# Kernel tuning notes

Measured on AMD Instinct MI355X. Metric: run time of the kernel, lower is better.

Reference implementation:

```python
import jax, jax.numpy as jnp
import numpy as np

N_WAY = 5
K_SHOT = 5
TEMPERATURE = 1.0
NEG = -1e9  # emulates 'column does not exist' for pad columns beyond umask_length
EPS = 1e-12  # matches torch F.normalize eps


def _l2n(x, axis):
    n = jnp.sqrt(jnp.sum(x * x, axis=axis, keepdims=True))
    return x / jnp.maximum(n, EPS)


def setup_inputs() -> dict:
    key = jax.random.key(0)
    k1, k2, k3, k4, k5 = jax.random.split(key, 5)
    b, c, h, w = 4, 64, 5, 5
    q, u = 75, 100
    support_xf = jax.random.normal(k1, (b, N_WAY * K_SHOT, c, h, w), jnp.float32)
    query_xf = jax.random.normal(k2, (b, q, c, h, w), jnp.float32)
    unlabeled_xf = jax.random.normal(k3, (b, u, c, h, w), jnp.float32)
    support_y = jax.random.randint(k4, (b, N_WAY * K_SHOT), 0, N_WAY)
    query_y = jax.random.randint(k5, (b, q), 0, N_WAY)
    return {"support_xf": support_xf, "support_y": support_y, "query_xf": query_xf,
            "query_y": query_y, "unlabeled_xf": unlabeled_xf}


def _forward(support_xf, query_xf, unlabeled_xf, query_y):
    b, q, c, h, w = query_xf.shape
    M_s = K_SHOT * h * w
    unl = unlabeled_xf.reshape(b, -1, c, h, w)
    u = unl.shape[1]
    M_u = u * h * w
    # pooled unlabeled local descriptors, flattened in (u, h, w) order -> [b, c, M_u]
    unl_feat = unl.transpose(0, 2, 1, 3, 4).reshape(b, c, M_u)
    # support -> [b, n_way, c, k_shot*h*w]
    sup = support_xf.reshape(b, N_WAY, K_SHOT, c, h, w).transpose(0, 1, 3, 2, 4, 5).reshape(b, N_WAY, c, M_s)
    # cosine similarity unlabeled -> support: [b, n_way, M_u, M_s]
    u2s = jnp.einsum('bwcn,bcm->bwmn', _l2n(sup, 2), _l2n(unl_feat, 1))
    pool = u2s.transpose(0, 2, 1, 3).reshape(b, M_u, N_WAY * M_s)
    s_nearest = jnp.argmax(pool, axis=1)          # per support loc: nearest unlabeled loc
    u_nearest = jnp.argmax(pool, axis=2)          # per unlabeled loc: nearest support loc
    mutual = jnp.take_along_axis(s_nearest, u_nearest, axis=1) == jnp.arange(M_u)[None, :]  # [b, M_u]
    # class with max similarity per unlabeled location
    cls = jnp.argmax(jnp.max(u2s, axis=-1), axis=1)  # [b, M_u]
    umask = jax.nn.one_hot(cls, N_WAY, dtype=jnp.float32).transpose(0, 2, 1) \
            * mutual[:, None, :].astype(jnp.float32)  # [b, n_way, M_u]
    counts = umask.sum(-1)                          # [b, n_way]
    L = counts.max()                                # umask_length (traced)
    # stream compaction via stable argsort of the 0/1 mask (preserves original order)
    order = jnp.argsort(-umask, axis=-1)            # jnp.argsort is stable
    pts = unl_feat.transpose(0, 2, 1)               # [b, M_u, c]
    gath = jnp.take_along_axis(pts[:, None, :, :], order[..., None], axis=2)  # [b, n_way, M_u, c]
    valid = (jnp.arange(M_u)[None, None, :] < counts[:, :, None]).astype(jnp.float32)
    comp = gath * valid[..., None]                  # rows beyond count are zeros (as in torch)
    s_cat = jnp.concatenate([sup, comp.transpose(0, 1, 3, 2)], axis=-1)  # [b, n_way, c, M_s+M_u]
    M_tot = M_s + M_u
    qn = _l2n(query_xf.reshape(b, q, c, h * w), 2)
    scn = _l2n(s_cat, 2)
    sim = jnp.einsum('bqcm,bwcn->bqwmn', qn, scn)   # [b, q, n_way, M_q, M_tot]
    sim = (sim + 1.0) * 0.5                          # FourLayer_64F branch
    # columns beyond umask_length don't exist in the torch dense tensor -> exclude from maxes
    pad = jnp.arange(M_tot)[None, None, None, None, :] >= (M_s + L)
    sim = jnp.where(pad, NEG, sim)
    M_q = h * w
    qm = sim.transpose(0, 1, 3, 2, 4).reshape(b, q, M_q, N_WAY * M_tot)
    support_nearest = jnp.argmax(qm, axis=2)        # [b, q, n_way*M_tot]
    query_nearest = jnp.argmax(qm, axis=3)          # [b, q, M_q]
    g = jnp.take_along_axis(support_nearest, query_nearest, axis=2)
    q_mask = (g == jnp.arange(M_q)[None, None, :]).astype(sim.dtype)  # mutual NN mask
    query_value = (jnp.max(sim, axis=-1) * q_mask[:, :, None, :]).sum(-1)  # [b, q, n_way]
    logits = query_value.reshape(b * q, N_WAY) / TEMPERATURE
    y = query_y.reshape(b * q)
    logp = jax.nn.log_softmax(logits, axis=-1)
    loss = -jnp.take_along_axis(logp, y[:, None], axis=1).mean()
    return loss


def reference(support_xf, support_y, query_xf, query_y, unlabeled_xf):
    return _forward(support_xf, query_xf, unlabeled_xf, query_y)
```

## Files before the change

### kernel.cpp

```cpp
#include <hip/hip_runtime.h>

#define NEGINF (-1e30f)

constexpr size_t OF_UNL  = 0;
constexpr size_t OF_SUP  = OF_UNL  + (size_t)4*2500*64;
constexpr size_t OF_SUPT = OF_SUP  + (size_t)4*5*125*64;
constexpr size_t OF_QT   = OF_SUPT + (size_t)4*5*64*128;
constexpr size_t OF_ROWV = OF_QT   + (size_t)300*28*64;
constexpr size_t OF_ROWI = OF_ROWV + (size_t)4*5*8*2500;
constexpr size_t OF_CVI  = OF_ROWI + (size_t)4*5*8*2500;
constexpr size_t OF_CMP  = OF_CVI  + (size_t)4*5*125*20*2;
constexpr size_t OF_CNT  = OF_CMP  + (size_t)4*5*2500;
constexpr size_t OF_UNEAR= OF_CNT  + 20;
constexpr size_t OF_SNEAR= OF_UNEAR+ 10000;
constexpr size_t OF_BV   = OF_SNEAR+ 2500;
constexpr size_t OF_BP   = OF_BV   + 37500;
constexpr size_t OF_AMX  = OF_BP   + 37500;

typedef __attribute__((ext_vector_type(4)))  float f4s;
typedef __attribute__((ext_vector_type(16))) float f16s;

__global__ __launch_bounds__(256) void knorm(
    const float* __restrict__ sup, const float* __restrict__ qry,
    const float* __restrict__ unl,
    float* __restrict__ unl_n, float* __restrict__ sup_n,
    float* __restrict__ supT, float* __restrict__ qt)
{
    int tid = threadIdx.x;
    int lane = tid & 63, wv = tid >> 6;
    int unit = blockIdx.x * 4 + wv;

    __shared__ float ls[4][1600];
    __shared__ float scl[4][32];

    const float* src;
    float* dstT;
    float* dst2 = nullptr;
    int dst2_shot = 0;
    bool isq = false;

    if (unit < 400) {
        int b = unit / 100, u = unit % 100;
        src  = unl + (size_t)unit * 1600;
        dstT = unl_n + ((size_t)(b * 2500 + u * 25)) * 64;
    } else if (unit < 500) {
        int idx2 = unit - 400;
        int b = idx2 / 25, r = idx2 % 25;
        int w = r / 5, shot = r % 5;
        src  = sup + (size_t)(b * 25 + r) * 1600;
        dstT = sup_n + ((size_t)(b * 625 + w * 125 + shot * 25)) * 64;
        dst2 = supT + ((size_t)(b * 5 + w) * 64) * 128;
        dst2_shot = shot * 25;
    } else {
        int bq = unit - 500;
        src  = qry + (size_t)bq * 1600;
        dstT = qt + (size_t)bq * 1792;
        isq = true;
    }

    const float4* s4 = (const float4*)src;
#pragma unroll
    for (int k = 0; k < 7; ++k) {
        int idx = k * 64 + lane;
        if (idx < 400) *(float4*)&ls[wv][idx * 4] = s4[idx];
    }
    __syncthreads();

    if (lane < 25) {
        int hw = lane;
        float p[16];
#pragma unroll
        for (int sub = 0; sub < 16; ++sub) {
            float s = 0.f;
#pragma unroll
            for (int j = 0; j < 4; ++j) {
                float v = ls[wv][(sub * 4 + j) * 25 + hw];
                s += v * v;
            }
            p[sub] = s;
        }
#pragma unroll
        for (int st = 1; st < 16; st <<= 1)
#pragma unroll
            for (int i = 0; i < 16; i += 2 * st)
                p[i] = p[i] + p[i + st];
        scl[wv][hw] = 1.f / fmaxf(sqrtf(p[0]), 1e-12f);
    }
    __syncthreads();

    float4* d4 = (float4*)dstT;
#pragma unroll
    for (int k = 0; k < 7; ++k) {
        int idx = k * 64 + lane;
        if (idx < 400) {
            int f = idx * 4;
            int r_ = f >> 6;
            int c0 = f & 63;
            float m = scl[wv][r_];
            float4 o;
            o.x = ls[wv][ c0      * 25 + r_] * m;
            o.y = ls[wv][(c0 + 1) * 25 + r_] * m;
            o.z = ls[wv][(c0 + 2) * 25 + r_] * m;
            o.w = ls[wv][(c0 + 3) * 25 + r_] * m;
            d4[idx] = o;
        }
    }
    if (isq) {
        if (lane < 48) d4[400 + lane] = make_float4(0.f, 0.f, 0.f, 0.f);
    }
    if (dst2) {
#pragma unroll
        for (int k = 0; k < 25; ++k) {
            int idx = k * 64 + lane;
            int c = idx / 25, hw2 = idx % 25;
            dst2[(size_t)c * 128 + dst2_shot + hw2] = ls[wv][idx] * scl[wv][hw2];
        }
    }
}

#define KB2(C) { \
    f16s s0, s1; \
    asm volatile("s_load_dwordx16 %0, %[b], %c[o0]\n\t" \
                 "s_load_dwordx16 %1, %[b], %c[o1]\n\t" \
                 "s_waitcnt lgkmcnt(0)" \
                 : "=s"(s0), "=s"(s1) \
                 : [b]"s"(sbp), [o0]"i"((C)*512), [o1]"i"((C)*512+512)); \
    float2 uv = *(const float2*)&uls[ml * 66 + (C)]; \
    acc[0]  = fmaf(uv.x, s0[0],  fmaf(uv.y, s1[0],  acc[0])); \
    acc[1]  = fmaf(uv.x, s0[1],  fmaf(uv.y, s1[1],  acc[1])); \
    acc[2]  = fmaf(uv.x, s0[2],  fmaf(uv.y, s1[2],  acc[2])); \
    acc[3]  = fmaf(uv.x, s0[3],  fmaf(uv.y, s1[3],  acc[3])); \
    acc[4]  = fmaf(uv.x, s0[4],  fmaf(uv.y, s1[4],  acc[4])); \
    acc[5]  = fmaf(uv.x, s0[5],  fmaf(uv.y, s1[5],  acc[5])); \
    acc[6]  = fmaf(uv.x, s0[6],  fmaf(uv.y, s1[6],  acc[6])); \
    acc[7]  = fmaf(uv.x, s0[7],  fmaf(uv.y, s1[7],  acc[7])); \
    acc[8]  = fmaf(uv.x, s0[8],  fmaf(uv.y, s1[8],  acc[8])); \
    acc[9]  = fmaf(uv.x, s0[9],  fmaf(uv.y, s1[9],  acc[9])); \
    acc[10] = fmaf(uv.x, s0[10], fmaf(uv.y, s1[10], acc[10])); \
    acc[11] = fmaf(uv.x, s0[11], fmaf(uv.y, s1[11], acc[11])); \
    acc[12] = fmaf(uv.x, s0[12], fmaf(uv.y, s1[12], acc[12])); \
    acc[13] = fmaf(uv.x, s0[13], fmaf(uv.y, s1[13], acc[13])); \
    acc[14] = fmaf(uv.x, s0[14], fmaf(uv.y, s1[14], acc[14])); \
    acc[15] = fmaf(uv.x, s0[15], fmaf(uv.y, s1[15], acc[15])); }
#define KB8(C) KB2(C) KB2((C)+2) KB2((C)+4) KB2((C)+6)

__global__ __launch_bounds__(256) void kb(
    const float* __restrict__ unl_n, const float* __restrict__ supT,
    float* __restrict__ rowv, int* __restrict__ rowi, float* __restrict__ colvi)
{
    int bid = blockIdx.x;
    int nc = bid & 3;
    int mb = (bid >> 2) % 20;
    int bw = bid / 80;
    int b  = bw / 5;
    int tid = threadIdx.x;
    int lane = tid & 63, wv = tid >> 6;

    __shared__ float uls[128 * 66];
    __shared__ float sv_[4][32];
    __shared__ int   si_[4][32];

    int m0 = mb * 128;
    int n0 = nc * 32;

    for (int i = tid; i < 128 * 16; i += 256) {
        int row = i >> 4, c4 = (i & 15) * 4;
        int m = m0 + row;
        float4 x = make_float4(0.f, 0.f, 0.f, 0.f);
        if (m < 2500) x = *(const float4*)(unl_n + ((size_t)(b * 2500 + m)) * 64 + c4);
        *(float2*)&uls[row * 66 + c4]     = make_float2(x.x, x.y);
        *(float2*)&uls[row * 66 + c4 + 2] = make_float2(x.z, x.w);
    }
    __syncthreads();

    int ml = tid & 127;
    int m  = m0 + ml;
    int nh = tid >> 7;
    int nbase = nh * 16;
    int nbu = __builtin_amdgcn_readfirstlane(nbase);
    int nn_total = (125 - n0) < 32 ? (125 - n0) : 32;
    const float* sbp = supT + ((size_t)bw * 64) * 128 + n0 + nbu;

    float acc[16];
#pragma unroll
    for (int j = 0; j < 16; ++j) acc[j] = 0.f;

    KB8(0)  KB8(8)  KB8(16) KB8(24)
    KB8(32) KB8(40) KB8(48) KB8(56)

    int nnloc = nn_total - nbase;
    nnloc = nnloc < 0 ? 0 : (nnloc > 16 ? 16 : nnloc);
    float rbv = NEGINF; int rbi = 0;
    for (int j = 0; j < nnloc; ++j)
        if (acc[j] > rbv) { rbv = acc[j]; rbi = n0 + nbase + j; }
    if (m < 2500) {
        int ck = nc * 2 + nh;
        rowv[((size_t)bw * 8 + ck) * 2500 + m] = rbv;
        rowi[((size_t)bw * 8 + ck) * 2500 + m] = rbi;
    }

#pragma unroll
    for (int j = 0; j < 16; ++j) {
        float v = (m < 2500 && (nbase + j) < nn_total) ? acc[j] : NEGINF;
        float vm = v;
#pragma unroll
        for (int s2 = 1; s2 < 64; s2 <<= 1) vm = fmaxf(vm, __shfl_xor(vm, s2));
        unsigned long long msk = __ballot(v == vm);
        int first = __ffsll((unsigned long long)msk) - 1;
        if (lane == 0) { sv_[wv][nbase + j] = vm; si_[wv][nbase + j] = m0 + (wv & 1) * 64 + first; }
    }
    __syncthreads();
    if (tid < nn_total) {
        int w0 = (tid < 16) ? 0 : 2;
        float v = sv_[w0][tid];     int vi = si_[w0][tid];
        float v2 = sv_[w0 + 1][tid]; int i2 = si_[w0 + 1][tid];
        if (v2 > v || (v2 == v && i2 < vi)) { v = v2; vi = i2; }
        float* cv = colvi + ((((size_t)bw) * 125 + (n0 + tid)) * 20 + mb) * 2;
        cv[0] = v; ((int*)cv)[1] = vi;
    }
}

__global__ __launch_bounds__(64) void kmerge(
    const float* __restrict__ rowv, const int* __restrict__ rowi,
    const float* __restrict__ colvi,
    int* __restrict__ unear, int* __restrict__ snear)
{
    int it = blockIdx.x * 64 + threadIdx.x;
    if (it < 10000) {
        int b = it / 2500, m = it % 2500;
        float bv = NEGINF; int bi = 0;
#pragma unroll
        for (int w = 0; w < 5; ++w) {
#pragma unroll
            for (int ck = 0; ck < 8; ++ck) {
                size_t o = (((size_t)(b * 5 + w)) * 8 + ck) * 2500 + m;
                float v = rowv[o];
                if (v > bv) { bv = v; bi = w * 125 + rowi[o]; }
            }
        }
        unear[it] = bi;
    } else if (it < 12500) {
        int idx = it - 10000;
        const float* p = colvi + (size_t)idx * 40;
        float bv = NEGINF; int bi = 0x7fffffff;
        for (int mb2 = 0; mb2 < 20; ++mb2) {
            float v = p[mb2 * 2]; int vi = ((const int*)p)[mb2 * 2 + 1];
            if (v > bv || (v == bv && vi < bi)) { bv = v; bi = vi; }
        }
        snear[idx] = bi;
    }
}

__global__ __launch_bounds__(256) void kcmp(
    const int* __restrict__ unear, const int* __restrict__ snear,
    int* __restrict__ cmp, int* __restrict__ cntg)
{
    int p = blockIdx.x;
    int b = p / 5, way = p % 5;
    int tid = threadIdx.x, lane = tid & 63, wv = tid >> 6;
    __shared__ unsigned long long masks[40];
    __shared__ int base[40];

    for (int ch = wv; ch < 40; ch += 4) {
        int m = ch * 64 + lane;
        bool ok = false;
        if (m < 2500) {
            int un = unear[b * 2500 + m];
            ok = (un / 125 == way) && (snear[b * 625 + un] == m);
        }
        unsigned long long msk = __ballot(ok ? 1 : 0);
        if (lane == 0) masks[ch] = msk;
    }
    __syncthreads();
    if (tid == 0) {
        int s = 0;
        for (int ch = 0; ch < 40; ++ch) { base[ch] = s; s += __popcll(masks[ch]); }
        cntg[p] = s;
    }
    __syncthreads();
    for (int ch = wv; ch < 40; ch += 4) {
        unsigned long long msk = masks[ch];
        if ((msk >> lane) & 1ull) {
            int pre = __popcll(msk & ((1ull << lane) - 1ull));
            cmp[(size_t)p * 2500 + base[ch] + pre] = ch * 64 + lane;
        }
    }
}

#define QLOAD(CG, Q0,Q1,Q2,Q3,Q4,Q5,Q6) \
  asm volatile( \
    "s_load_dwordx4 %0, %[b], %c[o0]\n\t" \
    "s_load_dwordx4 %1, %[b], %c[o1]\n\t" \
    "s_load_dwordx4 %2, %[b], %c[o2]\n\t" \
    "s_load_dwordx4 %3, %[b], %c[o3]\n\t" \
    "s_load_dwordx4 %4, %[b], %c[o4]\n\t" \
    "s_load_dwordx4 %5, %[b], %c[o5]\n\t" \
    "s_load_dwordx4 %6, %[b], %c[o6]\n\t" \
    "s_waitcnt lgkmcnt(0)" \
    : "=s"(Q0), "=s"(Q1), "=s"(Q2), "=s"(Q3), "=s"(Q4), "=s"(Q5), "=s"(Q6) \
    : [b]"s"(qbp), \
      [o0]"i"((CG)*16 + 0*256), [o1]"i"((CG)*16 + 1*256), \
      [o2]"i"((CG)*16 + 2*256), [o3]"i"((CG)*16 + 3*256), \
      [o4]"i"((CG)*16 + 4*256), [o5]"i"((CG)*16 + 5*256), \
      [o6]"i"((CG)*16 + 6*256))

#define CGSTEP(CG) { \
    f4s q0,q1,q2,q3,q4,q5,q6; \
    QLOAD(CG, q0,q1,q2,q3,q4,q5,q6); \
    float4 cl = *(const float4*)&cls[lane * 68 + (CG) * 4]; \
    acc[0]=fmaf(q0.x,cl.x,fmaf(q0.y,cl.y,fmaf(q0.z,cl.z,fmaf(q0.w,cl.w,acc[0])))); \
    acc[1]=fmaf(q1.x,cl.x,fmaf(q1.y,cl.y,fmaf(q1.z,cl.z,fmaf(q1.w,cl.w,acc[1])))); \
    acc[2]=fmaf(q2.x,cl.x,fmaf(q2.y,cl.y,fmaf(q2.z,cl.z,fmaf(q2.w,cl.w,acc[2])))); \
    acc[3]=fmaf(q3.x,cl.x,fmaf(q3.y,cl.y,fmaf(q3.z,cl.z,fmaf(q3.w,cl.w,acc[3])))); \
    acc[4]=fmaf(q4.x,cl.x,fmaf(q4.y,cl.y,fmaf(q4.z,cl.z,fmaf(q4.w,cl.w,acc[4])))); \
    acc[5]=fmaf(q5.x,cl.x,fmaf(q5.y,cl.y,fmaf(q5.z,cl.z,fmaf(q5.w,cl.w,acc[5])))); \
    acc[6]=fmaf(q6.x,cl.x,fmaf(q6.y,cl.y,fmaf(q6.z,cl.z,fmaf(q6.w,cl.w,acc[6])))); }

__global__ __launch_bounds__(256) void kc1(
    const float* __restrict__ qt, const float* __restrict__ sup_n,
    const float* __restrict__ unl_n, const int* __restrict__ cmp,
    const int* __restrict__ cntg,
    float* __restrict__ bvg, int* __restrict__ bpg,
    unsigned char* __restrict__ amaxg)
{
    int bid = blockIdx.x;
    int w = bid % 5, bq = bid / 5;
    int b = bq / 75;
    int tid = threadIdx.x;
    int lane = tid & 63;
    int wvu = __builtin_amdgcn_readfirstlane(tid >> 6);
    int pbw = b * 5 + w;

    int L = 0;
#pragma unroll
    for (int i = 0; i < 20; ++i) { int v = cntg[i]; L = L > v ? L : v; }
    int cntw = 0, wb = 0;
#pragma unroll
    for (int w2 = 0; w2 < 5; ++w2) {
        int c2 = cntg[b * 5 + w2];
        if (w2 < w) wb += 125 + c2;
        if (w2 == w) cntw = c2;
    }
    int cw = 125 + cntw;

    __shared__ float cls[64 * 68];
    __shared__ float amxv[4][64];
    __shared__ int   amxg_[4][64];
    __shared__ float redv[25];
    __shared__ int   redn[25];

    const float* qbp = qt + ((size_t)bq * 28 + wvu * 7) * 64;

    float rv[7]; int rn[7];
#pragma unroll
    for (int j = 0; j < 7; ++j) { rv[j] = NEGINF; rn[j] = 0x7fffffff; }

    int nb = (cw + 63) >> 6;

    for (int b4 = 0; b4 < nb; ++b4) {
        if (b4 > 0 && tid < 64) {
            int n = (b4 - 1) * 64 + tid;
            if (n < cw) {
                float v = amxv[0][tid]; int g = amxg_[0][tid];
#pragma unroll
                for (int g2 = 1; g2 < 4; ++g2)
                    if (amxv[g2][tid] > v) { v = amxv[g2][tid]; g = amxg_[g2][tid]; }
                amaxg[(size_t)bq * 3200 + (wb + n)] = (unsigned char)g;
            }
        }
#pragma unroll
        for (int k = 0; k < 4; ++k) {
            int i = tid + k * 256;
            int row = i >> 4, ch = i & 15;
            int n = b4 * 64 + row;
            float4 x = make_float4(0.f, 0.f, 0.f, 0.f);
            if (n < cw) {
                const float* cp;
                if (n < 125) cp = sup_n + (((size_t)pbw) * 125 + n) * 64;
                else { int m = cmp[((size_t)pbw) * 2500 + (n - 125)];
                       cp = unl_n + ((size_t)(b * 2500 + m)) * 64; }
                x = *(const float4*)(cp + ch * 4);
            }
            *(float4*)&cls[row * 68 + ch * 4] = x;
        }
        __syncthreads();

        float acc[7];
#pragma unroll
        for (int j = 0; j < 7; ++j) acc[j] = 0.f;

        CGSTEP(0);  CGSTEP(1);  CGSTEP(2);  CGSTEP(3);
        CGSTEP(4);  CGSTEP(5);  CGSTEP(6);  CGSTEP(7);
        CGSTEP(8);  CGSTEP(9);  CGSTEP(10); CGSTEP(11);
        CGSTEP(12); CGSTEP(13); CGSTEP(14); CGSTEP(15);

        bool colvalid = (b4 * 64 + lane) < cw;
        float cmax = NEGINF; int cam = 0;
#pragma unroll
        for (int j = 0; j < 7; ++j) {
            int mq = wvu * 7 + j;
            float s = (acc[j] + 1.0f) * 0.5f;
            float sm = (colvalid && mq < 25) ? s : NEGINF;
            if (sm > cmax) { cmax = sm; cam = mq; }
            float vm = sm;
#pragma unroll
            for (int t = 1; t < 64; t <<= 1) vm = fmaxf(vm, __shfl_xor(vm, t));
            unsigned long long msk = __ballot(sm == vm);
            int first = __ffsll(msk) - 1;
            if (vm > rv[j]) { rv[j] = vm; rn[j] = b4 * 64 + first; }
        }
        amxv[wvu][lane] = cmax; amxg_[wvu][lane] = cam;
        __syncthreads();
    }

    if (tid < 64) {
        int n = (nb - 1) * 64 + tid;
        if (n < cw) {
            float v = amxv[0][tid]; int g = amxg_[0][tid];
#pragma unroll
            for (int g2 = 1; g2 < 4; ++g2)
                if (amxv[g2][tid] > v) { v = amxv[g2][tid]; g = amxg_[g2][tid]; }
            amaxg[(size_t)bq * 3200 + (wb + n)] = (unsigned char)g;
        }
    }
    if (lane == 0) {
#pragma unroll
        for (int j = 0; j < 7; ++j) {
            int mq = wvu * 7 + j;
            if (mq < 25) { redv[mq] = rv[j]; redn[mq] = rn[j]; }
        }
    }
    __syncthreads();

    if (tid < 25) {
        float v = redv[tid]; int nn = redn[tid];
        int p = ((w * 2625 + nn) << 12) | (wb + nn);
        if (L > cntw) {
            int pp = ((w * 2625 + 125 + cntw) << 12) | 0xFFF;
            if (0.5f > v || (0.5f == v && pp < p)) { v = 0.5f; p = pp; }
        }
        size_t o = ((size_t)bq * 5 + w) * 25 + tid;
        bvg[o] = v; bpg[o] = p;
    }
}

__global__ __launch_bounds__(64) void kce(
    const float* __restrict__ bvg, const int* __restrict__ bpg,
    const unsigned char* __restrict__ amaxg, const int* __restrict__ qy,
    float* __restrict__ out)
{
    int bq = blockIdx.x;
    int tid = threadIdx.x;
    __shared__ float qmask[25];
    __shared__ float lg[5];
    if (tid < 25) {
        float v = NEGINF; int p = 0x7fffffff;
#pragma unroll
        for (int w = 0; w < 5; ++w) {
            size_t o = ((size_t)bq * 5 + w) * 25 + tid;
            float v2 = bvg[o]; int p2 = bpg[o];
            if (v2 > v || (v2 == v && p2 < p)) { v = v2; p = p2; }
        }
        int pos = p & 0xFFF;
        int g = (pos == 0xFFF) ? 0 : (int)amaxg[(size_t)bq * 3200 + pos];
        qmask[tid] = (g == tid) ? 1.0f : 0.0f;
    }
    __syncthreads();
    if (tid < 5) {
        float s = 0.f;
#pragma unroll
        for (int mq = 0; mq < 25; ++mq)
            s += bvg[((size_t)bq * 5 + tid) * 25 + mq] * qmask[mq];
        lg[tid] = s;
    }
    __syncthreads();
    if (tid == 0) {
        int y = qy[bq];
        float mx = lg[0];
#pragma unroll
        for (int w = 1; w < 5; ++w) mx = fmaxf(mx, lg[w]);
        float se = 0.f;
#pragma unroll
        for (int w = 0; w < 5; ++w) se += expf(lg[w] - mx);
        float loss = -(lg[y] - mx - logf(se));
        atomicAdd(out, loss * (1.0f / 300.0f));
    }
}

extern "C" void kernel_launch(void* const* d_in, const int* in_sizes, int n_in,
                              void* d_out, int out_size, void* d_ws, size_t ws_size,
                              hipStream_t stream)
{
    const float* sup = (const float*)d_in[0];
    const float* qry = (const float*)d_in[2];
    const int*   qy  = (const int*)d_in[3];
    const float* unl = (const float*)d_in[4];

    float* ws    = (float*)d_ws;
    float* unl_n = ws + OF_UNL;
    float* sup_n = ws + OF_SUP;
    float* supT  = ws + OF_SUPT;
    float* qt    = ws + OF_QT;
    float* rowv  = ws + OF_ROWV;
    int*   rowi  = (int*)(ws + OF_ROWI);
    float* colvi = ws + OF_CVI;
    int*   cmp   = (int*)(ws + OF_CMP);
    int*   cntg  = (int*)(ws + OF_CNT);
    int*   unear = (int*)(ws + OF_UNEAR);
    int*   snear = (int*)(ws + OF_SNEAR);
    float* bvg   = ws + OF_BV;
    int*   bpg   = (int*)(ws + OF_BP);
    unsigned char* amaxg = (unsigned char*)(ws + OF_AMX);

    hipMemsetAsync(d_out, 0, sizeof(float), stream);

    hipLaunchKernelGGL(knorm, dim3(200), dim3(256), 0, stream,
                       sup, qry, unl, unl_n, sup_n, supT, qt);
    hipLaunchKernelGGL(kb, dim3(1600), dim3(256), 0, stream,
                       unl_n, supT, rowv, rowi, colvi);
    hipLaunchKernelGGL(kmerge, dim3(196), dim3(64), 0, stream,
                       rowv, rowi, colvi, unear, snear);
    hipLaunchKernelGGL(kcmp, dim3(20), dim3(256), 0, stream,
                       unear, snear, cmp, cntg);
    hipLaunchKernelGGL(kc1, dim3(1500), dim3(256), 0, stream,
                       qt, sup_n, unl_n, cmp, cntg, bvg, bpg, amaxg);
    hipLaunchKernelGGL(kce, dim3(300), dim3(64), 0, stream,
                       bvg, bpg, amaxg, qy, (float*)d_out);
}
```

Baseline: 180.4 us.

## Replace merge and CE kernels with atomic packed-key argmax and last-block fusion

```diff
diff --git a/kernel.cpp b/kernel.cpp
--- a/kernel.cpp
+++ b/kernel.cpp
@@ -7,8 +7,10 @@
 constexpr size_t OF_SUPT = OF_SUP  + (size_t)4*5*125*64;
 constexpr size_t OF_QT   = OF_SUPT + (size_t)4*5*64*128;
 constexpr size_t OF_ROWV = OF_QT   + (size_t)300*28*64;
-constexpr size_t OF_ROWI = OF_ROWV + (size_t)4*5*8*2500;
-constexpr size_t OF_CVI  = OF_ROWI + (size_t)4*5*8*2500;
+constexpr size_t OF_UKEY = OF_ROWV;
+constexpr size_t OF_SKEY = OF_ROWV + 20000;
+constexpr size_t OF_CBQ  = OF_ROWV + 25000;
+constexpr size_t OF_CVI  = OF_ROWV + (size_t)2*4*5*8*2500;
 constexpr size_t OF_CMP  = OF_CVI  + (size_t)4*5*125*20*2;
 constexpr size_t OF_CNT  = OF_CMP  + (size_t)4*5*2500;
 constexpr size_t OF_UNEAR= OF_CNT  + 20;
@@ -20,24 +22,36 @@
 typedef __attribute__((ext_vector_type(4)))  float f4s;
 typedef __attribute__((ext_vector_type(16))) float f16s;
 
+__device__ __forceinline__ unsigned long long pack_key(float v, int idx) {
+    unsigned int e = __float_as_uint(v);
+    e ^= (e >> 31) ? 0xFFFFFFFFu : 0x80000000u;
+    return ((unsigned long long)e << 32) | (unsigned int)~idx;
+}
+
 __global__ __launch_bounds__(256) void knorm(
     const float* __restrict__ sup, const float* __restrict__ qry,
-    const float* __restrict__ unl,
-    float* __restrict__ unl_n, float* __restrict__ sup_n,
-    float* __restrict__ supT, float* __restrict__ qt)
+    const float* __restrict__ unl, float* __restrict__ ws,
+    float* __restrict__ out)
 {
+    float* unl_n = ws + OF_UNL;
+    float* sup_n = ws + OF_SUP;
+    float* supT  = ws + OF_SUPT;
+    float* qt    = ws + OF_QT;
+
     int tid = threadIdx.x;
     int lane = tid & 63, wv = tid >> 6;
+    int gid = blockIdx.x * 256 + tid;
+
+    if (gid == 0) *out = 0.f;
+    if (gid < 25300) ((unsigned int*)(ws + OF_UKEY))[gid] = 0u;
+
     int unit = blockIdx.x * 4 + wv;
 
     __shared__ float ls[4][1600];
     __shared__ float scl[4][32];
 
     const float* src;
-    float* dstT;
-    float* dst2 = nullptr;
-    int dst2_shot = 0;
-    bool isq = false;
+    float* dstT; float* dst2 = nullptr; int dst2_shot = 0; bool isq = false;
 
     if (unit < 400) {
         int b = unit / 100, u = unit % 100;
@@ -105,9 +119,7 @@
             d4[idx] = o;
         }
     }
-    if (isq) {
-        if (lane < 48) d4[400 + lane] = make_float4(0.f, 0.f, 0.f, 0.f);
-    }
+    if (isq && lane < 48) d4[400 + lane] = make_float4(0.f, 0.f, 0.f, 0.f);
     if (dst2) {
 #pragma unroll
         for (int k = 0; k < 25; ++k) {
@@ -146,13 +158,14 @@
 
 __global__ __launch_bounds__(256) void kb(
     const float* __restrict__ unl_n, const float* __restrict__ supT,
-    float* __restrict__ rowv, int* __restrict__ rowi, float* __restrict__ colvi)
+    unsigned long long* __restrict__ ukey, unsigned long long* __restrict__ skey)
 {
     int bid = blockIdx.x;
     int nc = bid & 3;
     int mb = (bid >> 2) % 20;
     int bw = bid / 80;
     int b  = bw / 5;
+    int w  = bw % 5;
     int tid = threadIdx.x;
     int lane = tid & 63, wv = tid >> 6;
 
@@ -193,11 +206,8 @@
     float rbv = NEGINF; int rbi = 0;
     for (int j = 0; j < nnloc; ++j)
         if (acc[j] > rbv) { rbv = acc[j]; rbi = n0 + nbase + j; }
-    if (m < 2500) {
-        int ck = nc * 2 + nh;
-        rowv[((size_t)bw * 8 + ck) * 2500 + m] = rbv;
-        rowi[((size_t)bw * 8 + ck) * 2500 + m] = rbi;
-    }
+    if (m < 2500)
+        atomicMax(ukey + (b * 2500 + m), pack_key(rbv, w * 125 + rbi));
 
 #pragma unroll
     for (int j = 0; j < 16; ++j) {
@@ -215,44 +225,13 @@
         float v = sv_[w0][tid];     int vi = si_[w0][tid];
         float v2 = sv_[w0 + 1][tid]; int i2 = si_[w0 + 1][tid];
         if (v2 > v || (v2 == v && i2 < vi)) { v = v2; vi = i2; }
-        float* cv = colvi + ((((size_t)bw) * 125 + (n0 + tid)) * 20 + mb) * 2;
-        cv[0] = v; ((int*)cv)[1] = vi;
+        atomicMax(skey + (bw * 125 + n0 + tid), pack_key(v, vi));
     }
 }
 
-__global__ __launch_bounds__(64) void kmerge(
-    const float* __restrict__ rowv, const int* __restrict__ rowi,
-    const float* __restrict__ colvi,
-    int* __restrict__ unear, int* __restrict__ snear)
-{
-    int it = blockIdx.x * 64 + threadIdx.x;
-    if (it < 10000) {
-        int b = it / 2500, m = it % 2500;
-        float bv = NEGINF; int bi = 0;
-#pragma unroll
-        for (int w = 0; w < 5; ++w) {
-#pragma unroll
-            for (int ck = 0; ck < 8; ++ck) {
-                size_t o = (((size_t)(b * 5 + w)) * 8 + ck) * 2500 + m;
-                float v = rowv[o];
-                if (v > bv) { bv = v; bi = w * 125 + rowi[o]; }
-            }
-        }
-        unear[it] = bi;
-    } else if (it < 12500) {
-        int idx = it - 10000;
-        const float* p = colvi + (size_t)idx * 40;
-        float bv = NEGINF; int bi = 0x7fffffff;
-        for (int mb2 = 0; mb2 < 20; ++mb2) {
-            float v = p[mb2 * 2]; int vi = ((const int*)p)[mb2 * 2 + 1];
-            if (v > bv || (v == bv && vi < bi)) { bv = v; bi = vi; }
-        }
-        snear[idx] = bi;
-    }
-}
-
 __global__ __launch_bounds__(256) void kcmp(
-    const int* __restrict__ unear, const int* __restrict__ snear,
+    const unsigned long long* __restrict__ ukey,
+    const unsigned long long* __restrict__ skey,
     int* __restrict__ cmp, int* __restrict__ cntg)
 {
     int p = blockIdx.x;
@@ -265,8 +244,9 @@
         int m = ch * 64 + lane;
         bool ok = false;
         if (m < 2500) {
-            int un = unear[b * 2500 + m];
-            ok = (un / 125 == way) && (snear[b * 625 + un] == m);
+            int un = (int)(~(unsigned int)ukey[b * 2500 + m]);
+            ok = (un / 125 == way) &&
+                 ((int)(~(unsigned int)skey[b * 625 + un]) == m);
         }
         unsigned long long msk = __ballot(ok ? 1 : 0);
         if (lane == 0) masks[ch] = msk;
@@ -321,7 +301,8 @@
     const float* __restrict__ unl_n, const int* __restrict__ cmp,
     const int* __restrict__ cntg,
     float* __restrict__ bvg, int* __restrict__ bpg,
-    unsigned char* __restrict__ amaxg)
+    unsigned char* __restrict__ amaxg, int* __restrict__ cntbq,
+    const int* __restrict__ qy, float* __restrict__ out)
 {
     int bid = blockIdx.x;
     int w = bid % 5, bq = bid / 5;
@@ -348,6 +329,9 @@
     __shared__ int   amxg_[4][64];
     __shared__ float redv[25];
     __shared__ int   redn[25];
+    __shared__ int   lastf;
+    __shared__ float qmask[25];
+    __shared__ float lg[5];
 
     const float* qbp = qt + ((size_t)bq * 28 + wvu * 7) * 64;
 
@@ -442,35 +426,41 @@
         size_t o = ((size_t)bq * 5 + w) * 25 + tid;
         bvg[o] = v; bpg[o] = p;
     }
-}
-
-__global__ __launch_bounds__(64) void kce(
-    const float* __restrict__ bvg, const int* __restrict__ bpg,
-    const unsigned char* __restrict__ amaxg, const int* __restrict__ qy,
-    float* __restrict__ out)
-{
-    int bq = blockIdx.x;
-    int tid = threadIdx.x;
-    __shared__ float qmask[25];
-    __shared__ float lg[5];
+
+    __syncthreads();
+    __threadfence();
+    if (tid == 0)
+        lastf = (__hip_atomic_fetch_add(cntbq + bq, 1, __ATOMIC_ACQ_REL,
+                                        __HIP_MEMORY_SCOPE_AGENT) == 4) ? 1 : 0;
+    __syncthreads();
+    if (!lastf) return;
+    __threadfence();
+
     if (tid < 25) {
         float v = NEGINF; int p = 0x7fffffff;
 #pragma unroll
-        for (int w = 0; w < 5; ++w) {
-            size_t o = ((size_t)bq * 5 + w) * 25 + tid;
-            float v2 = bvg[o]; int p2 = bpg[o];
+        for (int w2 = 0; w2 < 5; ++w2) {
+            size_t o = ((size_t)bq * 5 + w2) * 25 + tid;
+            float v2 = __hip_atomic_load(&bvg[o], __ATOMIC_RELAXED, __HIP_MEMORY_SCOPE_AGENT);
+            int   p2 = __hip_atomic_load(&bpg[o], __ATOMIC_RELAXED, __HIP_MEMORY_SCOPE_AGENT);
             if (v2 > v || (v2 == v && p2 < p)) { v = v2; p = p2; }
         }
         int pos = p & 0xFFF;
-        int g = (pos == 0xFFF) ? 0 : (int)amaxg[(size_t)bq * 3200 + pos];
+        int g = 0;
+        if (pos != 0xFFF)
+            g = (int)__hip_atomic_load(&amaxg[(size_t)bq * 3200 + pos],
+                                       __ATOMIC_RELAXED, __HIP_MEMORY_SCOPE_AGENT);
         qmask[tid] = (g == tid) ? 1.0f : 0.0f;
     }
     __syncthreads();
     if (tid < 5) {
         float s = 0.f;
 #pragma unroll
-        for (int mq = 0; mq < 25; ++mq)
-            s += bvg[((size_t)bq * 5 + tid) * 25 + mq] * qmask[mq];
+        for (int mq = 0; mq < 25; ++mq) {
+            size_t o = ((size_t)bq * 5 + tid) * 25 + mq;
+            float v2 = __hip_atomic_load(&bvg[o], __ATOMIC_RELAXED, __HIP_MEMORY_SCOPE_AGENT);
+            s += v2 * qmask[mq];
+        }
         lg[tid] = s;
     }
     __syncthreads();
@@ -478,10 +468,10 @@
         int y = qy[bq];
         float mx = lg[0];
 #pragma unroll
-        for (int w = 1; w < 5; ++w) mx = fmaxf(mx, lg[w]);
+        for (int w2 = 1; w2 < 5; ++w2) mx = fmaxf(mx, lg[w2]);
         float se = 0.f;
 #pragma unroll
-        for (int w = 0; w < 5; ++w) se += expf(lg[w] - mx);
+        for (int w2 = 0; w2 < 5; ++w2) se += expf(lg[w2] - mx);
         float loss = -(lg[y] - mx - logf(se));
         atomicAdd(out, loss * (1.0f / 300.0f));
     }
@@ -501,29 +491,22 @@
     float* sup_n = ws + OF_SUP;
     float* supT  = ws + OF_SUPT;
     float* qt    = ws + OF_QT;
-    float* rowv  = ws + OF_ROWV;
-    int*   rowi  = (int*)(ws + OF_ROWI);
-    float* colvi = ws + OF_CVI;
+    unsigned long long* ukey = (unsigned long long*)(ws + OF_UKEY);
+    unsigned long long* skey = (unsigned long long*)(ws + OF_SKEY);
+    int*   cntbq = (int*)(ws + OF_CBQ);
     int*   cmp   = (int*)(ws + OF_CMP);
     int*   cntg  = (int*)(ws + OF_CNT);
-    int*   unear = (int*)(ws + OF_UNEAR);
-    int*   snear = (int*)(ws + OF_SNEAR);
     float* bvg   = ws + OF_BV;
     int*   bpg   = (int*)(ws + OF_BP);
     unsigned char* amaxg = (unsigned char*)(ws + OF_AMX);
 
-    hipMemsetAsync(d_out, 0, sizeof(float), stream);
-
     hipLaunchKernelGGL(knorm, dim3(200), dim3(256), 0, stream,
-                       sup, qry, unl, unl_n, sup_n, supT, qt);
+                       sup, qry, unl, ws, (float*)d_out);
     hipLaunchKernelGGL(kb, dim3(1600), dim3(256), 0, stream,
-                       unl_n, supT, rowv, rowi, colvi);
-    hipLaunchKernelGGL(kmerge, dim3(196), dim3(64), 0, stream,
-                       rowv, rowi, colvi, unear, snear);
+                       unl_n, supT, ukey, skey);
     hipLaunchKernelGGL(kcmp, dim3(20), dim3(256), 0, stream,
-                       unear, snear, cmp, cntg);
+                       ukey, skey, cmp, cntg);
     hipLaunchKernelGGL(kc1, dim3(1500), dim3(256), 0, stream,
-                       qt, sup_n, unl_n, cmp, cntg, bvg, bpg, amaxg);
-    hipLaunchKernelGGL(kce, dim3(300), dim3(64), 0, stream,
-                       bvg, bpg, amaxg, qy, (float*)d_out);
+                       qt, sup_n, unl_n, cmp, cntg, bvg, bpg, amaxg,
+                       cntbq, qy, (float*)d_out);
 }
```

Result: slower. 286.8 us (+58.9%).
